# Optimization experiments

Measured on AMD Instinct MI355X. Metric: run time of the kernel, lower is better.

Reference implementation:

```python
import jax, jax.numpy as jnp
import numpy as np

PRECS = 1e-6
# [min, max] scaling ranges for the 12 XAJ parameters (order matches parameters[:, i, :])
PARA_SCALE = [[0.3, 2.0], [0.0, 5.0], [0.01, 100.0], [0.01, 100.0], [0.01, 200.0],
              [0.09, 1.0], [0.01, 100.0], [0.0, 10.0], [0.01, 0.7], [0.01, 0.7],
              [0.0, 0.998], [0.0, 0.998]]


def setup_inputs() -> dict:
    key = jax.random.key(0)
    k1, k2 = jax.random.split(key)
    Nstep, Ngrid, mu = 365, 2000, 8
    # col 0 = P (mm/d), col 2 = PET (mm/d); col 1 unused by the model
    x = jax.random.uniform(k1, (Nstep, Ngrid, 3), dtype=jnp.float32) * 10.0
    parameters = jax.random.uniform(k2, (Ngrid, 12, mu), dtype=jnp.float32)
    return {"x": x, "parameters": parameters, "mu": mu}


def _xaj(x, parameters, mu):
    P = x[:, :, 0]          # [T, Ngrid]
    PET = x[:, :, 2]        # [T, Ngrid]  (index 2, matching the original code)
    Ngrid = x.shape[1]

    sc = lambda a, i: PARA_SCALE[i][0] + a * (PARA_SCALE[i][1] - PARA_SCALE[i][0])
    (parKE, parB, parWUM, parWLM, parWM, parC, parSM, parEX,
     parKI_, parKG_, parCI, parCG) = [sc(parameters[:, i, :], i) for i in range(12)]

    wdm = jnp.maximum(parWM - parWUM - parWLM, 0.0)
    sum_k = parKI_ + parKG_
    parKI = jnp.where(sum_k < 1.0, parKI_, (1.0 - PRECS) * parKI_ / (sum_k + PRECS))
    parKG = jnp.where(sum_k < 1.0, parKG_, (1.0 - PRECS) * parKG_ / (sum_k + PRECS))

    init_state = jnp.full((Ngrid, mu), 0.001, dtype=jnp.float32)
    WU0 = WL0 = WD0 = S0 = QI0 = QG0 = FR0_init = init_state

    def step(carry, inp):
        WU, WL, WD, S, FR0, QI, QG = carry
        P_row, PET_row = inp                      # each [Ngrid]
        P_t = P_row[:, None]                      # broadcast over mu
        PET_t = PET_row[:, None] * parKE

        # three-layer evapotranspiration
        EU = jnp.minimum(PET_t, WU + P_t)
        D = jnp.maximum(PET_t - EU, 0.0)
        wet_excess = jnp.maximum(WL - parC * parWLM, 0.0)
        wet_ratio = wet_excess / (wet_excess + 1.0)
        EL_wet = D * WL / (parWLM + PRECS)
        EL_dry = jnp.minimum(parC * D, WL)
        EL = jnp.maximum(wet_ratio * EL_wet + (1.0 - wet_ratio) * EL_dry, 0.0)
        EL = jnp.minimum(EL, WL)
        D_res = jnp.maximum(D - EL, 0.0)
        ED = jnp.minimum(parC * D_res, WD)
        E = EU + EL + ED

        # saturation-excess runoff
        PE = jnp.maximum(P_t - E, 0.0)
        W = WU + WL + WD
        WMM = parWM * (1.0 + parB)
        base_W = jnp.maximum(1.0 - W / (parWM + PRECS), PRECS)
        A = WMM * (1.0 - base_W ** (1.0 / (1.0 + parB)))
        ratio = jnp.minimum((PE + A) / (WMM + PRECS), 1.0)
        R_per = jnp.where(PE + A < WMM,
                          PE - (parWM - W) + parWM * (1.0 - ratio) ** (1.0 + parB),
                          PE - (parWM - W))
        R_per = jnp.maximum(R_per, 0.0)

        # soil moisture update (fill top-down, deplete top-down)
        dW = P_t - E - R_per
        dpos = jnp.maximum(dW, 0.0)
        fill_u = jnp.minimum(dpos, jnp.maximum(parWUM - WU, 0.0))
        WU = WU + fill_u; dpos = dpos - fill_u
        fill_l = jnp.minimum(dpos, jnp.maximum(parWLM - WL, 0.0))
        WL = WL + fill_l; dpos = dpos - fill_l
        fill_d = jnp.minimum(dpos, jnp.maximum(wdm - WD, 0.0))
        WD = WD + fill_d
        dneg = jnp.maximum(-dW, 0.0)
        sub_u = jnp.minimum(dneg, WU)
        WU = WU - sub_u; dneg = dneg - sub_u
        sub_l = jnp.minimum(dneg, WL)
        WL = WL - sub_l; dneg = dneg - sub_l
        sub_d = jnp.minimum(dneg, WD)
        WD = WD - sub_d

        # free-water reservoir + three-flow separation
        FR_new = R_per / (PE + PRECS)
        FR = jnp.where(PE > 0.0, FR_new, FR0)
        FR = jnp.clip(FR, 0.0, 1.0)
        S_eq = jnp.minimum(S * FR0 / (FR + PRECS), parSM)
        SMM = parSM * (1.0 + parEX)
        ratio_s = jnp.maximum(1.0 - S_eq / (parSM + PRECS), PRECS)
        AU = SMM * (1.0 - ratio_s ** (1.0 / (1.0 + parEX)))
        ratio_pa = jnp.minimum((PE + AU) / (SMM + PRECS), 1.0)
        RS1 = (PE + S_eq - parSM + parSM * (1.0 - ratio_pa) ** (1.0 + parEX)) * FR
        RS2 = (PE + S_eq - parSM) * FR
        RS = jnp.where(PE + AU < SMM, RS1, RS2)
        RS = jnp.minimum(jnp.maximum(RS, 0.0), R_per)
        S = jnp.minimum(S_eq + (R_per - RS) / (FR + PRECS), parSM)
        RI = parKI * S * FR
        RG = parKG * S * FR
        S = S * (1.0 - parKI - parKG)

        # linear reservoirs
        QI = parCI * QI + (1.0 - parCI) * RI
        QG = parCG * QG + (1.0 - parCG) * RG

        return (WU, WL, WD, S, FR, QI, QG), (RS, QI, QG, E)

    carry0 = (WU0, WL0, WD0, S0, FR0_init, QI0, QG0)
    _, (QS_inflow, QI_inflow, QG_inflow, ET_series) = jax.lax.scan(step, carry0, (P, PET))

    QSave = QS_inflow.mean(-1, keepdims=True)
    QIave = QI_inflow.mean(-1, keepdims=True)
    QGave = QG_inflow.mean(-1, keepdims=True)
    ETave = ET_series.mean(-1, keepdims=True)
    river_inflow = QS_inflow + QI_inflow + QG_inflow
    Qs = river_inflow.mean(-1, keepdims=True)   # muwts is None
    # [Nstep, Ngrid, 5]
    return jnp.concatenate([Qs, QSave, QIave, QGave, ETave], axis=-1)


def reference(x, parameters, mu):
    return _xaj(x, parameters, mu)
```

## Files before the change

### kernel.cpp

```cpp
#include <hip/hip_runtime.h>

#define PRECS 1e-6f

__device__ __forceinline__ float fpow(float b, float e) {
    return __builtin_amdgcn_exp2f(e * __builtin_amdgcn_logf(b));
}

__device__ __forceinline__ float frcp(float v) {
    return __builtin_amdgcn_rcpf(v);
}

template <int CTRL>
__device__ __forceinline__ float dpp_mov(float v) {
    return __int_as_float(
        __builtin_amdgcn_update_dpp(0, __float_as_int(v), CTRL, 0xF, 0xF, true));
}

__device__ __forceinline__ float rsum8(float v) {
    v += dpp_mov<0xB1>(v);
    v += dpp_mov<0x4E>(v);
    v += dpp_mov<0x141>(v);
    return v;
}

__global__ __launch_bounds__(256, 1) void xaj_kernel(
    const float* __restrict__ x,
    const float* __restrict__ prm,
    float* __restrict__ out)
{
    constexpr int Nstep = 365, Ngrid = 2000;
    constexpr int xstride = Ngrid * 3;
    constexpr int K = 16;
    constexpr int NBLK = 23;
    constexpr int NPH  = NBLK + 3;

    const int wid  = (int)threadIdx.x >> 6;
    const int lane = (int)threadIdx.x & 63;
    const int g = blockIdx.x * 8 + (lane >> 3);
    const int m = lane & 7;

    __shared__ float2 stIn[2][K][64];
    __shared__ float4 stA[4][K][64];
    __shared__ float2 stFR[2][K][64];
    __shared__ float2 stB[2][K][64];

    const float lo[12] = {0.3f,0.0f,0.01f,0.01f,0.01f,0.09f,0.01f,0.0f,0.01f,0.01f,0.0f,0.0f};
    const float hi[12] = {2.0f,5.0f,100.0f,100.0f,200.0f,1.0f,100.0f,10.0f,0.7f,0.7f,0.998f,0.998f};
    float p[12];
    const float* pb = prm + (size_t)g * 96 + m;
#pragma unroll
    for (int i = 0; i < 12; ++i)
        p[i] = lo[i] + pb[i * 8] * (hi[i] - lo[i]);

    const float KE=p[0], B=p[1], WUM=p[2], WLM=p[3], WM=p[4], C=p[5],
                SM=p[6], EX=p[7], KI_=p[8], KG_=p[9], CI=p[10], CG=p[11];

    const float wdm  = fmaxf(WM - WUM - WLM, 0.f);
    const float sumk = KI_ + KG_;
    const float nrm  = (1.f - PRECS) / (sumk + PRECS);
    const float KI   = (sumk < 1.f) ? KI_ : KI_ * nrm;
    const float KG   = (sumk < 1.f) ? KG_ : KG_ * nrm;
    const float expB = 1.f + B,  invB  = 1.f / expB;
    const float WMM  = WM * expB;
    const float expEX= 1.f + EX, invEX = 1.f / expEX;
    const float SMM  = SM * expEX;
    const float inv_WLM = 1.f / (WLM + PRECS);
    const float inv_WM  = 1.f / (WM  + PRECS);
    const float inv_WMM = 1.f / (WMM + PRECS);
    const float inv_SM  = 1.f / (SM  + PRECS);
    const float inv_SMM = 1.f / (SMM + PRECS);
    const float oneK = 1.f - KI - KG;
    const float omCI = 1.f - CI, omCG = 1.f - CG;
    const float CWLM = C * WLM;
    const float inv1p = 1.f / (1.f + PRECS);
    const float eps2  = fmaxf(PRECS, fmaf(-SM, inv_SM, 1.f));

    float WU = 0.001f, WL = 0.001f, WD = 0.001f;
    float S = 0.001f, FR0 = 0.001f;
    float iFR0 = frcp(FR0 + PRECS);
    float QI = 0.001f, QG = 0.001f;
    const float cKI = omCI * KI, cKG = omCG * KG;
    const float wa = (m == 0 || m == 1) ? 0.125f : 0.f;
    const float wb = (m == 0 || m == 2) ? 0.125f : 0.f;
    const float wc = (m == 0 || m == 3) ? 0.125f : 0.f;
    const float wd = (m >= 4) ? 0.125f : 0.f;
    const int   col = (m < 4) ? m : 4;
    float* outp = out + (size_t)g * 5 + col;
    const size_t ostr = (size_t)Ngrid * 5;
    const float* xg = x + (size_t)g * 3;
    float Pr[K], Er[K];

    auto ASTEP = [&](int buf, int obuf) {
        float2 rin[K];
#pragma unroll
        for (int k = 0; k < K; ++k)
            rin[k] = stIn[buf][k][lane];
#pragma unroll
        for (int k = 0; k < K; ++k) {
            const float Pt = rin[k].x, PET_t = rin[k].y;
            const float EU = fminf(PET_t, WU + Pt);
            const float D  = fmaxf(PET_t - Pt - WU, 0.f);
            const float we = fmaxf(WL - CWLM, 0.f);
            const float wr = we * frcp(we + 1.f);
            const float cwet = wr * WL * inv_WLM;
            const float ELdry = fminf(C * D, WL);
            const float EL = fminf(fmaxf(fmaf(1.f - wr, ELdry, cwet * D), 0.f), WL);
            const float ED = fminf(C * fmaxf(D - EL, 0.f), WD);
            const float E  = EU + EL + ED;
            const float PE = fmaxf(Pt - E, 0.f);
            const float W = WU + WL + WD;
            const float base_W = fmaxf(fmaf(-W, inv_WM, 1.f), PRECS);
            const float pw1 = fpow(base_W, invB);
            const float omr = fmaxf(fmaf(-PE, inv_WMM, pw1), 0.f);
            const float R_per = fmaxf(fmaf(WM, fpow(omr, expB), PE + (W - WM)), 0.f);
            const float dW = Pt - E - R_per;
            const float capD = fmaxf(wdm, WD);
            const float cum0 = WU + dW;
            const float WUn  = __builtin_amdgcn_fmed3f(cum0, 0.f, WUM);
            const float cum1 = WL + (cum0 - WUn);
            const float WLn  = __builtin_amdgcn_fmed3f(cum1, 0.f, WLM);
            const float cum2 = WD + (cum1 - WLn);
            const float WDn  = __builtin_amdgcn_fmed3f(cum2, 0.f, capD);
            WU = WUn; WL = WLn; WD = WDn;
            stA[obuf][k][lane] = make_float4(PE, R_per, E, 0.f);
        }
    };

    auto BSTEP = [&](int abuf, int fbuf) {
        float4 ra[K];
        float2 rf[K];
#pragma unroll
        for (int k = 0; k < K; ++k) ra[k] = stA[abuf][k][lane];
#pragma unroll
        for (int k = 0; k < K; ++k) rf[k] = stFR[fbuf][k][lane];
#pragma unroll
        for (int k = 0; k < K; ++k) {
            const float PE = ra[k].x, R_per = ra[k].y;
            const bool wet = PE > 0.f;
            const float FR  = wet ? rf[k].x : FR0;
            const float iFR = wet ? rf[k].y : iFR0;
            const float sf  = S * FR0;
            const float sf2 = sf * inv_SM;
            const float S_eq = fminf(sf * iFR, SM);
            const float ratio_s = fmaxf(fmaf(-sf2, iFR, 1.f), eps2);
            const float u   = fpow(ratio_s, invEX);
            const float om2 = fmaxf(fmaf(-PE, inv_SMM, u), 0.f);
            const float base = (PE - SM) + S_eq;
            float RS = fmaf(SM, fpow(om2, expEX), base) * FR;
            RS = __builtin_amdgcn_fmed3f(RS, 0.f, R_per);
            const float Sn = fminf(fmaf(R_per - RS, iFR, S_eq), SM);
            S  = Sn * oneK;
            FR0 = FR; iFR0 = iFR;
            stB[fbuf][k][lane] = make_float2(RS, FR * Sn);
        }
    };

    auto CISSUE = [&](int blk) {
#pragma unroll
        for (int k = 0; k < K; ++k) {
            int t = blk * K + k;
            t = (t < Nstep) ? t : Nstep - 1;
            const float* xq = xg + (size_t)t * xstride;
            Pr[k] = xq[0];
            Er[k] = xq[2];
        }
    };
    auto CFR = [&](int abuf, int fbuf) {
#pragma unroll
        for (int k = 0; k < K; ++k) {
            const float4 ra = stA[abuf][k][lane];
            const float q  = frcp(ra.x + PRECS);
            const float aa = ra.y * q;
            stFR[fbuf][k][lane] =
                make_float2(fminf(aa, 1.f), fmaxf(frcp(aa + PRECS), inv1p));
        }
    };
    auto CWRITE = [&](int buf) {
#pragma unroll
        for (int k = 0; k < K; ++k)
            stIn[buf][k][lane] = make_float2(Pr[k], Er[k] * KE);
    };

    auto DSTEP = [&](int bbuf, int abuf, int blk) {
        float2 rb[K];
        float  re[K];
#pragma unroll
        for (int k = 0; k < K; ++k) rb[k] = stB[bbuf][k][lane];
#pragma unroll
        for (int k = 0; k < K; ++k) re[k] = stA[abuf][k][lane].z;
        const int t0 = blk * K;
#pragma unroll
        for (int k = 0; k < K; ++k) {
            QI = fmaf(CI, QI, cKI * rb[k].y);
            QG = fmaf(CG, QG, cKG * rb[k].y);
            const float u0 = rsum8(rb[k].x);
            const float u1 = rsum8(QI);
            const float u2 = rsum8(QG);
            const float u3 = rsum8(re[k]);
            const float v = fmaf(u0, wa, fmaf(u1, wb, fmaf(u2, wc, u3 * wd)));
            if (t0 + k < Nstep)
                outp[(size_t)(t0 + k) * ostr] = v;
        }
    };

    if (wid == 2) { CISSUE(0); CWRITE(0); }
    __syncthreads();

#pragma unroll 1
    for (int ph = 0; ph < NPH; ++ph) {
        if (wid == 0) {
            if (ph < NBLK) ASTEP(ph & 1, ph & 3);
        } else if (wid == 1) {
            if (ph >= 2 && ph < NBLK + 2) BSTEP((ph - 2) & 3, (ph - 2) & 1);
        } else if (wid == 2) {
            const bool ld = (ph + 1 < NBLK);
            if (ld) CISSUE(ph + 1);
            if (ph >= 1 && ph < NBLK + 1)
                CFR((ph - 1) & 3, (ph - 1) & 1);
            if (ld) CWRITE((ph + 1) & 1);
        } else {
            if (ph >= 3) DSTEP((ph - 3) & 1, (ph - 3) & 3, ph - 3);
        }
        __syncthreads();
    }
}

extern "C" void kernel_launch(void* const* d_in, const int* in_sizes, int n_in,
                              void* d_out, int out_size, void* d_ws, size_t ws_size,
                              hipStream_t stream) {
    const float* x   = (const float*)d_in[0];
    const float* prm = (const float*)d_in[1];
    float* out = (float*)d_out;
    xaj_kernel<<<250, 256, 0, stream>>>(x, prm, out);
}
```

Baseline: 58.29 us.

## Move FR carry selection to loader wave and shorten serial A/B chains

The wet/dry FR selection and the oneK*FR0 factor move out of the serial B recurrence into the loader wave's CFR pass, which now emits FR, 1/FR and a scale factor for B. B keeps an unscaled S carry, and A tracks the total W incrementally with a clamp instead of summing three layers. E is forwarded through stB so D no longer reads stA. The goal is to shorten the loop-carried dependency chains in the A and B waves, at the cost of wider LDS records and possible small numerical differences in the incremental W.

```diff
diff --git a/kernel.cpp b/kernel.cpp
--- a/kernel.cpp
+++ b/kernel.cpp
@@ -41,8 +41,8 @@
 
     __shared__ float2 stIn[2][K][64];
     __shared__ float4 stA[4][K][64];
-    __shared__ float2 stFR[2][K][64];
-    __shared__ float2 stB[2][K][64];
+    __shared__ float4 stFR[2][K][64];
+    __shared__ float4 stB[2][K][64];
 
     const float lo[12] = {0.3f,0.0f,0.01f,0.01f,0.01f,0.09f,0.01f,0.0f,0.01f,0.01f,0.0f,0.0f};
     const float hi[12] = {2.0f,5.0f,100.0f,100.0f,200.0f,1.0f,100.0f,10.0f,0.7f,0.7f,0.998f,0.998f};
@@ -73,11 +73,13 @@
     const float omCI = 1.f - CI, omCG = 1.f - CG;
     const float CWLM = C * WLM;
     const float inv1p = 1.f / (1.f + PRECS);
+    const float sumUL = WUM + WLM;
     const float eps2  = fmaxf(PRECS, fmaf(-SM, inv_SM, 1.f));
 
     float WU = 0.001f, WL = 0.001f, WD = 0.001f;
-    float S = 0.001f, FR0 = 0.001f;
-    float iFR0 = frcp(FR0 + PRECS);
+    float W  = 0.001f + 0.001f + 0.001f;
+    float Snc = 0.001f / oneK;
+    float FRc = 0.001f, iFRc = frcp(0.001f + PRECS);
     float QI = 0.001f, QG = 0.001f;
     const float cKI = omCI * KI, cKG = omCG * KG;
     const float wa = (m == 0 || m == 1) ? 0.125f : 0.f;
@@ -90,11 +92,11 @@
     const float* xg = x + (size_t)g * 3;
     float Pr[K], Er[K];
 
-    auto ASTEP = [&](int buf, int obuf) {
+    auto ASTEP = [&](int ibuf, int obuf) {
         float2 rin[K];
 #pragma unroll
         for (int k = 0; k < K; ++k)
-            rin[k] = stIn[buf][k][lane];
+            rin[k] = stIn[ibuf][k][lane];
 #pragma unroll
         for (int k = 0; k < K; ++k) {
             const float Pt = rin[k].x, PET_t = rin[k].y;
@@ -108,50 +110,44 @@
             const float ED = fminf(C * fmaxf(D - EL, 0.f), WD);
             const float E  = EU + EL + ED;
             const float PE = fmaxf(Pt - E, 0.f);
-            const float W = WU + WL + WD;
             const float base_W = fmaxf(fmaf(-W, inv_WM, 1.f), PRECS);
             const float pw1 = fpow(base_W, invB);
             const float omr = fmaxf(fmaf(-PE, inv_WMM, pw1), 0.f);
             const float R_per = fmaxf(fmaf(WM, fpow(omr, expB), PE + (W - WM)), 0.f);
             const float dW = Pt - E - R_per;
             const float capD = fmaxf(wdm, WD);
-            const float cum0 = WU + dW;
-            const float WUn  = __builtin_amdgcn_fmed3f(cum0, 0.f, WUM);
-            const float cum1 = WL + (cum0 - WUn);
-            const float WLn  = __builtin_amdgcn_fmed3f(cum1, 0.f, WLM);
-            const float cum2 = WD + (cum1 - WLn);
-            const float WDn  = __builtin_amdgcn_fmed3f(cum2, 0.f, capD);
+            W = __builtin_amdgcn_fmed3f(W + dW, 0.f, sumUL + capD);
+            const float c0  = WU + dW;
+            const float WUn = __builtin_amdgcn_fmed3f(c0, 0.f, WUM);
+            const float c1  = WL + (c0 - WUn);
+            const float WLn = __builtin_amdgcn_fmed3f(c1, 0.f, WLM);
+            const float c2  = WD + (c1 - WLn);
+            const float WDn = __builtin_amdgcn_fmed3f(c2, 0.f, capD);
             WU = WUn; WL = WLn; WD = WDn;
             stA[obuf][k][lane] = make_float4(PE, R_per, E, 0.f);
         }
     };
 
     auto BSTEP = [&](int abuf, int fbuf) {
-        float4 ra[K];
-        float2 rf[K];
+        float4 ra[K], rg[K];
 #pragma unroll
         for (int k = 0; k < K; ++k) ra[k] = stA[abuf][k][lane];
 #pragma unroll
-        for (int k = 0; k < K; ++k) rf[k] = stFR[fbuf][k][lane];
+        for (int k = 0; k < K; ++k) rg[k] = stFR[fbuf][k][lane];
 #pragma unroll
         for (int k = 0; k < K; ++k) {
             const float PE = ra[k].x, R_per = ra[k].y;
-            const bool wet = PE > 0.f;
-            const float FR  = wet ? rf[k].x : FR0;
-            const float iFR = wet ? rf[k].y : iFR0;
-            const float sf  = S * FR0;
-            const float sf2 = sf * inv_SM;
+            const float FR = rg[k].x, iFR = rg[k].y;
+            const float sf = Snc * rg[k].z;
             const float S_eq = fminf(sf * iFR, SM);
-            const float ratio_s = fmaxf(fmaf(-sf2, iFR, 1.f), eps2);
+            const float ratio_s = fmaxf(fmaf(-(sf * inv_SM), iFR, 1.f), eps2);
             const float u   = fpow(ratio_s, invEX);
             const float om2 = fmaxf(fmaf(-PE, inv_SMM, u), 0.f);
             const float base = (PE - SM) + S_eq;
             float RS = fmaf(SM, fpow(om2, expEX), base) * FR;
             RS = __builtin_amdgcn_fmed3f(RS, 0.f, R_per);
-            const float Sn = fminf(fmaf(R_per - RS, iFR, S_eq), SM);
-            S  = Sn * oneK;
-            FR0 = FR; iFR0 = iFR;
-            stB[fbuf][k][lane] = make_float2(RS, FR * Sn);
+            Snc = fminf(fmaf(R_per - RS, iFR, S_eq), SM);
+            stB[fbuf][k][lane] = make_float4(RS, FR * Snc, ra[k].z, 0.f);
         }
     };
 
@@ -169,10 +165,15 @@
 #pragma unroll
         for (int k = 0; k < K; ++k) {
             const float4 ra = stA[abuf][k][lane];
+            const float gk = oneK * FRc;
             const float q  = frcp(ra.x + PRECS);
             const float aa = ra.y * q;
-            stFR[fbuf][k][lane] =
-                make_float2(fminf(aa, 1.f), fmaxf(frcp(aa + PRECS), inv1p));
+            const float FRn  = fminf(aa, 1.f);
+            const float iFRn = fmaxf(frcp(aa + PRECS), inv1p);
+            const bool wet = ra.x > 0.f;
+            FRc  = wet ? FRn  : FRc;
+            iFRc = wet ? iFRn : iFRc;
+            stFR[fbuf][k][lane] = make_float4(FRc, iFRc, gk, 0.f);
         }
     };
     auto CWRITE = [&](int buf) {
@@ -181,13 +182,10 @@
             stIn[buf][k][lane] = make_float2(Pr[k], Er[k] * KE);
     };
 
-    auto DSTEP = [&](int bbuf, int abuf, int blk) {
-        float2 rb[K];
-        float  re[K];
+    auto DSTEP = [&](int bbuf, int blk) {
+        float4 rb[K];
 #pragma unroll
         for (int k = 0; k < K; ++k) rb[k] = stB[bbuf][k][lane];
-#pragma unroll
-        for (int k = 0; k < K; ++k) re[k] = stA[abuf][k][lane].z;
         const int t0 = blk * K;
 #pragma unroll
         for (int k = 0; k < K; ++k) {
@@ -196,7 +194,7 @@
             const float u0 = rsum8(rb[k].x);
             const float u1 = rsum8(QI);
             const float u2 = rsum8(QG);
-            const float u3 = rsum8(re[k]);
+            const float u3 = rsum8(rb[k].z);
             const float v = fmaf(u0, wa, fmaf(u1, wb, fmaf(u2, wc, u3 * wd)));
             if (t0 + k < Nstep)
                 outp[(size_t)(t0 + k) * ostr] = v;
@@ -219,7 +217,7 @@
                 CFR((ph - 1) & 3, (ph - 1) & 1);
             if (ld) CWRITE((ph + 1) & 1);
         } else {
-            if (ph >= 3) DSTEP((ph - 3) & 1, (ph - 3) & 3, ph - 3);
+            if (ph >= 3) DSTEP((ph - 3) & 1, ph - 3);
         }
         __syncthreads();
     }
```

After: 60.02 us. 1.03x slower.
